# Kernel optimization log

Hardware: AMD Instinct MI355X
Metric: run time of the kernel (lower is better)

Reference implementation:

```python
import jax, jax.numpy as jnp
import numpy as np
from jax import lax

G, NPER, K = 64, 1024, 512          # graphs, nodes per graph, kept per graph (ceil(0.5*1024))
N, E = G * NPER, 1_048_576          # total nodes, total edges
F, H, C = 128, 128, 10              # in_feats, hidden_dim, num_classes


def gcn(x, src, dst, ew, W, b, num_nodes):
    """PyG GCNConv: D^{-1/2}(A+I)D^{-1/2} X W + b, with edge weights ew."""
    xw = x @ W                                              # [N, H]
    deg = jax.ops.segment_sum(ew, dst, num_segments=num_nodes) + 1.0  # +1 self loop
    dinv = lax.rsqrt(deg)
    coef = dinv[src] * dinv[dst] * ew                       # [E]
    agg = jax.ops.segment_sum(coef[:, None] * xw[src], dst, num_segments=num_nodes)
    return agg + (dinv * dinv)[:, None] * xw + b            # self-loop term + bias


def setup_inputs() -> dict:
    key = jax.random.key(0)
    ks = jax.random.split(key, 10)
    x = jax.random.normal(ks[0], (N, F), jnp.float32)
    # intra-graph random edges: dst forced into same graph block as src
    src = jax.random.randint(ks[1], (E,), 0, N, dtype=jnp.int32)
    dst = (src // NPER) * NPER + jax.random.randint(ks[2], (E,), 0, NPER, dtype=jnp.int32)
    edge_index = jnp.stack([src, dst])                      # [2, E]
    batch = jnp.repeat(jnp.arange(G, dtype=jnp.int32), NPER)
    W1 = jax.random.normal(ks[3], (F, H), jnp.float32) / np.sqrt(F)
    b1 = jnp.zeros((H,), jnp.float32)
    p = jax.random.normal(ks[4], (H,), jnp.float32) / np.sqrt(H)   # TopKPooling score vector
    W2 = jax.random.normal(ks[5], (H, H), jnp.float32) / np.sqrt(H)
    b2 = jnp.zeros((H,), jnp.float32)
    Wl = jax.random.normal(ks[6], (H, C), jnp.float32) / np.sqrt(H)
    bl = jnp.zeros((C,), jnp.float32)
    return dict(x=x, edge_index=edge_index, batch=batch, W1=W1, b1=b1, p=p, W2=W2, b2=b2, Wl=Wl, bl=bl)


def reference(x, edge_index, batch, W1, b1, p, W2, b2, Wl, bl):
    src, dst = edge_index[0], edge_index[1]
    ew1 = jnp.ones((E,), x.dtype)
    h = jax.nn.relu(gcn(x, src, dst, ew1, W1, b1, N))       # conv1 + relu

    # --- TopKPooling: score = tanh(x.p/||p||), keep top-K per graph, gate x by score ---
    score = jnp.tanh((h @ p) / jnp.linalg.norm(p))          # [N]
    vals, idx = lax.top_k(score.reshape(G, NPER), K)        # per-graph top-k, [G, K]
    perm = (idx + jnp.arange(G, dtype=idx.dtype)[:, None] * NPER).reshape(-1)  # global ids [G*K]
    h2 = h[perm] * vals.reshape(-1, 1)                      # gated kept nodes [G*K, H]

    # edge re-index: keep only edges with both endpoints surviving (mask via weight 0)
    new_id = jnp.full((N,), -1, jnp.int32).at[perm].set(jnp.arange(G * K, dtype=jnp.int32))
    s2, d2 = new_id[src], new_id[dst]
    mask = (s2 >= 0) & (d2 >= 0)
    ew2 = mask.astype(h.dtype)
    s2 = jnp.where(mask, s2, 0)
    d2 = jnp.where(mask, d2, 0)

    h3 = jax.nn.relu(gcn(h2, s2, d2, ew2, W2, b2, G * K))   # conv2 + relu

    pooled = h3.reshape(G, K, H).mean(axis=1)               # global_mean_pool (equal counts)
    return pooled @ Wl + bl                                 # [G, C]
```

## Files before the change

### kernel.cpp

```cpp
#include <hip/hip_runtime.h>

#define NNODES 65536
#define NEDGES 1048576
#define NGRAPH 64
#define NPERG  1024
#define KEEP   512
#define M2     (NGRAPH * KEEP)
#define HD     128
#define NC     10
#define EMAX   20480

#define OW1 0
#define OW2 16384
#define OWL 32768
#define OB1 34048
#define OB2 34176
#define OP  34304
#define OBL 34432
#define NCVT 34448

typedef __attribute__((ext_vector_type(8))) short bf16x8;
typedef __attribute__((ext_vector_type(4))) float f32x4;

__device__ __forceinline__ float bf2f(unsigned short u) {
    return __uint_as_float(((unsigned int)u) << 16);
}
__device__ __forceinline__ unsigned short f2bf(float f) {
    unsigned int u = __float_as_uint(f);
    unsigned int r = (u + 0x7FFFu + ((u >> 16) & 1u)) >> 16;
    return (unsigned short)r;
}

__global__ __launch_bounds__(256) void prep_kernel(
    const void* __restrict__ W1, const void* __restrict__ b1, const void* __restrict__ p,
    const void* __restrict__ W2, const void* __restrict__ b2, const void* __restrict__ Wl,
    const void* __restrict__ bl, int* __restrict__ flag, float* __restrict__ cw,
    float* __restrict__ invnorm, int* __restrict__ new_id, int* __restrict__ ghist,
    int* __restrict__ gcur0, float* __restrict__ pooled,
    unsigned short* __restrict__ w1t, unsigned short* __restrict__ w2t) {
    int bid = blockIdx.x, t = threadIdx.x;
    const unsigned short* w1u = (const unsigned short*)W1;
    int local = 0;
    for (int i = t; i < 512; i += 256) {
        unsigned short u = w1u[2 * i];
        int e = (u >> 7) & 0xFF;
        local += (e >= 100 && e <= 140) ? 1 : 0;
    }
    __shared__ int red[256];
    red[t] = local;
    __syncthreads();
    for (int off = 128; off; off >>= 1) {
        if (t < off) red[t] += red[t + off];
        __syncthreads();
    }
    int fl = (red[0] >= 384) ? 1 : 0;
    if (bid == 0 && t == 0) flag[0] = fl;

    if (bid < 135) {
        int gid = bid * 256 + t;
        if (gid < NCVT) {
            const void* srcp; int idx;
            if (gid < OB1) {
                if (gid < OW2)      { srcp = W1; idx = gid - OW1; }
                else if (gid < OWL) { srcp = W2; idx = gid - OW2; }
                else                { srcp = Wl; idx = gid - OWL; }
            } else {
                if (gid < OB2)      { srcp = b1; idx = gid - OB1; }
                else if (gid < OP)  { srcp = b2; idx = gid - OB2; }
                else if (gid < OBL) { srcp = p;  idx = gid - OP; }
                else                { srcp = bl; idx = gid - OBL; }
            }
            float v;
            if (gid >= OWL && gid < OB1 && idx >= 1280) v = 0.f;
            else if (gid >= OBL && idx >= NC) v = 0.f;
            else if (fl) v = bf2f(((const unsigned short*)srcp)[idx]);
            else v = ((const float*)srcp)[idx];
            cw[gid] = v;
            if (gid < OW2) {
                int k = gid >> 7, n = gid & 127;
                w1t[n * 128 + k] = f2bf(v);
            } else if (gid < OWL) {
                int r = gid - OW2;
                int k = r >> 7, n = r & 127;
                w2t[n * 128 + k] = f2bf(v);
            }
        }
    } else if (bid == 135) {
        __shared__ float s2a[128];
        float pv = 0.f;
        if (t < 128) pv = fl ? bf2f(((const unsigned short*)p)[t]) : ((const float*)p)[t];
        if (t < 128) s2a[t] = pv * pv;
        __syncthreads();
        for (int off = 64; off; off >>= 1) {
            if (t < off) s2a[t] += s2a[t + off];
            __syncthreads();
        }
        if (t == 0) invnorm[0] = 1.0f / sqrtf(s2a[0]);
    } else {
        int i = (bid - 136) * 256 + t;
        new_id[i] = -1;
        if (i < NGRAPH) { ghist[i] = 0; gcur0[i] = 0; }
        if (i < NGRAPH * HD) pooled[i] = 0.f;
    }
}

__global__ __launch_bounds__(256) void hist_kernel(const int* __restrict__ src,
                                                   int* __restrict__ ghist) {
    __shared__ int lh[NGRAPH];
    int tid = threadIdx.x;
    if (tid < NGRAPH) lh[tid] = 0;
    __syncthreads();
    int e0 = blockIdx.x * 4096;
    for (int k = 0; k < 16; k++) atomicAdd(&lh[src[e0 + k * 256 + tid] >> 10], 1);
    __syncthreads();
    if (tid < NGRAPH) atomicAdd(&ghist[tid], lh[tid]);
}
__global__ __launch_bounds__(256) void binpass_kernel(const int* __restrict__ src,
                                                      const int* __restrict__ dst,
                                                      const int* __restrict__ ghist,
                                                      int* __restrict__ gcur0,
                                                      unsigned int* __restrict__ elist) {
    __shared__ int gh[NGRAPH];
    __shared__ int gbS[NGRAPH];
    __shared__ int lh[NGRAPH];
    __shared__ int lbase[NGRAPH];
    int tid = threadIdx.x;
    if (tid < NGRAPH) { gh[tid] = ghist[tid]; lh[tid] = 0; }
    __syncthreads();
    if (tid == 0) {
        int s = 0;
        for (int i = 0; i < NGRAPH; i++) { gbS[i] = s; s += gh[i]; }
    }
    __syncthreads();
    int e0 = blockIdx.x * 4096;
    int gs[16]; unsigned int pk[16];
    for (int k = 0; k < 16; k++) {
        int e = e0 + k * 256 + tid;
        int s = src[e], d = dst[e];
        gs[k] = s >> 10;
        pk[k] = (unsigned)(s & 1023) | ((unsigned)(d & 1023) << 10);
        atomicAdd(&lh[gs[k]], 1);
    }
    __syncthreads();
    if (tid < NGRAPH) { lbase[tid] = gbS[tid] + atomicAdd(&gcur0[tid], lh[tid]); lh[tid] = 0; }
    __syncthreads();
    for (int k = 0; k < 16; k++) {
        int g = gs[k];
        int pos = lbase[g] + atomicAdd(&lh[g], 1);
        elist[pos] = pk[k];
    }
}

__global__ __launch_bounds__(1024) void csr_sort_kernel(
    const unsigned int* __restrict__ elist, const int* __restrict__ ghist,
    unsigned short* __restrict__ csr16, int* __restrict__ node_base,
    int* __restrict__ deg_out, float* __restrict__ dinv_out) {
    __shared__ unsigned short sc[EMAX];
    __shared__ int cnt[NPERG];
    __shared__ int cur[NPERG];
    __shared__ int wsum[16];
    __shared__ int gh[NGRAPH];
    __shared__ int baseS, nS;
    int g = blockIdx.x, t = threadIdx.x;
    cnt[t] = 0;
    if (t < NGRAPH) gh[t] = ghist[t];
    __syncthreads();
    if (t == 0) {
        int s = 0;
        for (int i = 0; i < g; i++) s += gh[i];
        baseS = s; nS = gh[g];
    }
    __syncthreads();
    int base = baseS;
    int n = nS; if (n > EMAX) n = EMAX;
    for (int j = t; j < n; j += 1024) atomicAdd(&cnt[(elist[base + j] >> 10) & 1023], 1);
    __syncthreads();
    int v = cnt[t];
    int lane = t & 63;
    int x = v;
    for (int off = 1; off < 64; off <<= 1) {
        int y = __shfl_up(x, off);
        if (lane >= off) x += y;
    }
    if (lane == 63) wsum[t >> 6] = x;
    __syncthreads();
    if (t < 16) {
        int wv = wsum[t];
        int wx = wv;
        for (int off = 1; off < 16; off <<= 1) {
            int y = __shfl_up(wx, off);
            if (t >= off) wx += y;
        }
        wsum[t] = wx - wv;
    }
    __syncthreads();
    int excl = x - v + wsum[t >> 6];
    cur[t] = excl;
    deg_out[g * NPERG + t] = v;
    dinv_out[g * NPERG + t] = rsqrtf((float)v + 1.0f);
    node_base[g * NPERG + t] = base + excl;
    __syncthreads();
    for (int j = t; j < n; j += 1024) {
        unsigned int pk = elist[base + j];
        int d = (pk >> 10) & 1023;
        int pos = atomicAdd(&cur[d], 1);
        sc[pos] = (unsigned short)(pk & 1023);
    }
    __syncthreads();
    for (int j = t; j < n; j += 1024) csr16[base + j] = sc[j];
}

__global__ __launch_bounds__(256) void gemm_a_kernel(const void* __restrict__ Araw,
                                                     const unsigned short* __restrict__ Wtb,
                                                     unsigned int* __restrict__ Cb,
                                                     const int* __restrict__ flag) {
    int tid = threadIdx.x;
    int row0 = blockIdx.x * 64;
    int wave = tid >> 6, lane = tid & 63;
    int r0 = row0 + wave * 16;
    int row = r0 + (lane & 15);
    int ko = (lane >> 4) * 8;
    f32x4 acc[8];
#pragma unroll
    for (int c = 0; c < 8; c++) acc[c] = (f32x4){0.f, 0.f, 0.f, 0.f};
    bf16x8 afr[4];
    if (flag[0]) {
        const unsigned short* arow = (const unsigned short*)Araw + (size_t)row * HD + ko;
#pragma unroll
        for (int kk = 0; kk < 4; kk++) afr[kk] = *(const bf16x8*)(arow + kk * 32);
    } else {
        const float* arow = (const float*)Araw + (size_t)row * HD + ko;
#pragma unroll
        for (int kk = 0; kk < 4; kk++) {
            float4 f0 = *(const float4*)(arow + kk * 32);
            float4 f1 = *(const float4*)(arow + kk * 32 + 4);
            bf16x8 a;
            a[0] = (short)f2bf(f0.x); a[1] = (short)f2bf(f0.y);
            a[2] = (short)f2bf(f0.z); a[3] = (short)f2bf(f0.w);
            a[4] = (short)f2bf(f1.x); a[5] = (short)f2bf(f1.y);
            a[6] = (short)f2bf(f1.z); a[7] = (short)f2bf(f1.w);
            afr[kk] = a;
        }
    }
    const unsigned short* brow = Wtb + (lane & 15) * HD + ko;
#pragma unroll
    for (int kk = 0; kk < 4; kk++) {
#pragma unroll
        for (int c = 0; c < 8; c++) {
            bf16x8 b = *(const bf16x8*)(brow + c * 16 * HD + kk * 32);
            acc[c] = __builtin_amdgcn_mfma_f32_16x16x32_bf16(afr[kk], b, acc[c], 0, 0, 0);
        }
    }
    int orow0 = r0 + (lane >> 4) * 4;
    bool even = !(lane & 1);
#pragma unroll
    for (int c = 0; c < 8; c++) {
#pragma unroll
        for (int j = 0; j < 4; j++) {
            float v = acc[c][j];
            float pt = __shfl_xor(v, 1);
            if (even) {
                unsigned int u = (unsigned int)f2bf(v) | ((unsigned int)f2bf(pt) << 16);
                Cb[(size_t)(orow0 + j) * 64 + ((c * 16 + (lane & 15)) >> 1)] = u;
            }
        }
    }
}

__global__ __launch_bounds__(256) void s1_pull(const unsigned short* __restrict__ csr16,
                                               const int* __restrict__ node_base,
                                               const int* __restrict__ deg,
                                               const float* __restrict__ dinv,
                                               const unsigned int* __restrict__ xwb,
                                               const float* __restrict__ b1,
                                               const float* __restrict__ pvec,
                                               const float* __restrict__ invnorm,
                                               float* __restrict__ h,
                                               float* __restrict__ score) {
    int b = blockIdx.x;
    int xcd = b & 7, j = b >> 3;
    int g = (j >> 8) * 8 + xcd;
    int n = g * NPERG + (j & 255) * 4 + (threadIdx.x >> 6);
    int lane = threadIdx.x & 63;
    int gb = g * NPERG;
    int base = node_base[n], cnt = deg[n];
    int e = 0; float ds = 0.f;
    if (lane < cnt) {
        e = csr16[base + lane];
        ds = dinv[gb + e];
    }
    float a0 = 0.f, a1 = 0.f;
    int klim = cnt < 64 ? cnt : 64;
    int k = 0;
    for (; k + 3 < klim; k += 4) {
        int s0 = __shfl(e, k), s1 = __shfl(e, k + 1);
        int s2 = __shfl(e, k + 2), s3 = __shfl(e, k + 3);
        float d0 = __shfl(ds, k), d1 = __shfl(ds, k + 1);
        float d2 = __shfl(ds, k + 2), d3 = __shfl(ds, k + 3);
        unsigned int u0 = xwb[(size_t)(gb + s0) * 64 + lane];
        unsigned int u1 = xwb[(size_t)(gb + s1) * 64 + lane];
        unsigned int u2 = xwb[(size_t)(gb + s2) * 64 + lane];
        unsigned int u3 = xwb[(size_t)(gb + s3) * 64 + lane];
        a0 += d0 * __uint_as_float(u0 << 16); a1 += d0 * __uint_as_float(u0 & 0xFFFF0000u);
        a0 += d1 * __uint_as_float(u1 << 16); a1 += d1 * __uint_as_float(u1 & 0xFFFF0000u);
        a0 += d2 * __uint_as_float(u2 << 16); a1 += d2 * __uint_as_float(u2 & 0xFFFF0000u);
        a0 += d3 * __uint_as_float(u3 << 16); a1 += d3 * __uint_as_float(u3 & 0xFFFF0000u);
    }
    for (; k < klim; k++) {
        int sk = __shfl(e, k);
        float dk = __shfl(ds, k);
        unsigned int u = xwb[(size_t)(gb + sk) * 64 + lane];
        a0 += dk * __uint_as_float(u << 16); a1 += dk * __uint_as_float(u & 0xFFFF0000u);
    }
    for (; k < cnt; k++) {
        int sk = csr16[base + k];
        float dk = dinv[gb + sk];
        unsigned int u = xwb[(size_t)(gb + sk) * 64 + lane];
        a0 += dk * __uint_as_float(u << 16); a1 += dk * __uint_as_float(u & 0xFFFF0000u);
    }
    float dn = dinv[n];
    float self = dn * dn;
    unsigned int us = xwb[(size_t)n * 64 + lane];
    float2 bb = ((const float2*)b1)[lane];
    float h0 = fmaxf(dn * a0 + self * __uint_as_float(us << 16) + bb.x, 0.f);
    float h1 = fmaxf(dn * a1 + self * __uint_as_float(us & 0xFFFF0000u) + bb.y, 0.f);
    float2 ho = {h0, h1};
    ((float2*)h)[(size_t)n * 64 + lane] = ho;
    float2 pp = ((const float2*)pvec)[lane];
    float sv = h0 * pp.x + h1 * pp.y;
    for (int off = 32; off; off >>= 1) sv += __shfl_down(sv, off);
    if (lane == 0) score[n] = tanhf(sv * invnorm[0]);
}

__global__ __launch_bounds__(1024) void topk_kernel(const float* __restrict__ score,
                                                    const unsigned int* __restrict__ elist,
                                                    const int* __restrict__ ghist,
                                                    float* __restrict__ vals,
                                                    int* __restrict__ perm,
                                                    int* __restrict__ new_id,
                                                    float* __restrict__ dinv2) {
    __shared__ float sv[1024];
    __shared__ int si[1024];
    __shared__ short nid[1024];
    __shared__ int d2[KEEP];
    __shared__ int gh[NGRAPH];
    __shared__ int baseS, nS;
    int g = blockIdx.x, t = threadIdx.x;
    sv[t] = score[g * NPERG + t];
    si[t] = t;
    nid[t] = -1;
    if (t < KEEP) d2[t] = 0;
    if (t < NGRAPH) gh[t] = ghist[t];
    __syncthreads();
    if (t == 0) {
        int s = 0;
        for (int i = 0; i < g; i++) s += gh[i];
        baseS = s; nS = gh[g];
    }
    for (int k = 2; k <= 1024; k <<= 1) {
        for (int j = k >> 1; j > 0; j >>= 1) {
            int l = t ^ j;
            if (l > t) {
                bool desc = ((t & k) == 0);
                float va = sv[t], vb = sv[l];
                int ia = si[t], ib = si[l];
                bool gab = (va > vb) || (va == vb && ia < ib);
                if (gab != desc) { sv[t] = vb; si[t] = ib; sv[l] = va; si[l] = ia; }
            }
            __syncthreads();
        }
    }
    if (t < KEEP) {
        int node = g * NPERG + si[t];
        int slot = g * KEEP + t;
        vals[slot] = sv[t];
        perm[slot] = node;
        new_id[node] = slot;
        nid[si[t]] = (short)t;
    }
    __syncthreads();
    int base = baseS, n = nS;
    for (int j = t; j < n; j += 1024) {
        unsigned int pk = elist[base + j];
        int s = pk & 1023, d = (pk >> 10) & 1023;
        short ns = nid[s], nd = nid[d];
        if (ns >= 0 && nd >= 0) atomicAdd(&d2[nd], 1);
    }
    __syncthreads();
    if (t < KEEP) dinv2[g * KEEP + t] = rsqrtf((float)d2[t] + 1.0f);
}

__global__ __launch_bounds__(256) void gemm_gather(const float* __restrict__ h,
                                                   const int* __restrict__ perm,
                                                   const float* __restrict__ vals,
                                                   const unsigned short* __restrict__ Wtb,
                                                   float* __restrict__ C) {
    int tid = threadIdx.x;
    int row0 = blockIdx.x * 64;
    int wave = tid >> 6, lane = tid & 63;
    int r0 = row0 + wave * 16;
    int m = r0 + (lane & 15);
    int ko = (lane >> 4) * 8;
    float sc = vals[m];
    const float* arow = h + (size_t)perm[m] * HD + ko;
    bf16x8 afr[4];
#pragma unroll
    for (int kk = 0; kk < 4; kk++) {
        float4 f0 = *(const float4*)(arow + kk * 32);
        float4 f1 = *(const float4*)(arow + kk * 32 + 4);
        bf16x8 a;
        a[0] = (short)f2bf(f0.x * sc); a[1] = (short)f2bf(f0.y * sc);
        a[2] = (short)f2bf(f0.z * sc); a[3] = (short)f2bf(f0.w * sc);
        a[4] = (short)f2bf(f1.x * sc); a[5] = (short)f2bf(f1.y * sc);
        a[6] = (short)f2bf(f1.z * sc); a[7] = (short)f2bf(f1.w * sc);
        afr[kk] = a;
    }
    f32x4 acc[8];
#pragma unroll
    for (int c = 0; c < 8; c++) acc[c] = (f32x4){0.f, 0.f, 0.f, 0.f};
    const unsigned short* brow = Wtb + (lane & 15) * HD + ko;
#pragma unroll
    for (int kk = 0; kk < 4; kk++) {
#pragma unroll
        for (int c = 0; c < 8; c++) {
            bf16x8 b = *(const bf16x8*)(brow + c * 16 * HD + kk * 32);
            acc[c] = __builtin_amdgcn_mfma_f32_16x16x32_bf16(afr[kk], b, acc[c], 0, 0, 0);
        }
    }
    int orow0 = r0 + (lane >> 4) * 4;
    bool even = !(lane & 1);
    float2* C2 = (float2*)C;
#pragma unroll
    for (int c = 0; c < 8; c++) {
#pragma unroll
        for (int j = 0; j < 4; j++) {
            float v = acc[c][j];
            float pt = __shfl_xor(v, 1);
            if (even) {
                float2 o = {v, pt};
                C2[(size_t)(orow0 + j) * 64 + ((c * 16 + (lane & 15)) >> 1)] = o;
            }
        }
    }
}

__global__ __launch_bounds__(256) void s2_pull(const unsigned short* __restrict__ csr16,
                                               const int* __restrict__ node_base,
                                               const int* __restrict__ deg,
                                               const int* __restrict__ perm,
                                               const int* __restrict__ new_id,
                                               const float* __restrict__ dinv2,
                                               const float* __restrict__ xw2,
                                               const float* __restrict__ b2,
                                               float* __restrict__ pooled) {
    __shared__ float pr[HD];
    __shared__ int cnk[4][64];
    __shared__ float cds[4][64];
    int tid = threadIdx.x;
    if (tid < HD) pr[tid] = 0.f;
    __syncthreads();
    int b = blockIdx.x;
    int xcd = b & 7, j = b >> 3;
    int g = (j >> 7) * 8 + xcd;
    int wv = tid >> 6;
    int m = g * KEEP + (j & 127) * 4 + wv;
    int lane = tid & 63;
    int node = perm[m];
    int gb = node & ~(NPERG - 1);
    int base = node_base[node], cnt = deg[node];
    int nk = 0; float ds = 0.f;
    if (lane < cnt) {
        int ns = new_id[gb + csr16[base + lane]];
        if (ns >= 0) { nk = ns; ds = dinv2[ns]; }
    }
    unsigned long long msk = __ballot(ds != 0.f);
    int pos = __popcll(msk & ((1ull << lane) - 1ull));
    if (ds != 0.f) { cnk[wv][pos] = nk; cds[wv][pos] = ds; }
    int na = __popcll(msk);
    const float2* xf2 = (const float2*)xw2;
    float a0 = 0.f, a1 = 0.f;
    int k = 0;
    for (; k + 3 < na; k += 4) {
        int s0 = cnk[wv][k], s1 = cnk[wv][k + 1];
        int s2 = cnk[wv][k + 2], s3 = cnk[wv][k + 3];
        float d0 = cds[wv][k], d1 = cds[wv][k + 1];
        float d2 = cds[wv][k + 2], d3 = cds[wv][k + 3];
        float2 v0 = xf2[(size_t)s0 * 64 + lane];
        float2 v1 = xf2[(size_t)s1 * 64 + lane];
        float2 v2 = xf2[(size_t)s2 * 64 + lane];
        float2 v3 = xf2[(size_t)s3 * 64 + lane];
        a0 += d0 * v0.x; a1 += d0 * v0.y;
        a0 += d1 * v1.x; a1 += d1 * v1.y;
        a0 += d2 * v2.x; a1 += d2 * v2.y;
        a0 += d3 * v3.x; a1 += d3 * v3.y;
    }
    for (; k < na; k++) {
        int sk = cnk[wv][k];
        float dk = cds[wv][k];
        float2 v = xf2[(size_t)sk * 64 + lane];
        a0 += dk * v.x; a1 += dk * v.y;
    }
    for (int kk = 64; kk < cnt; kk++) {
        int ns = new_id[gb + csr16[base + kk]];
        if (ns >= 0) {
            float dk = dinv2[ns];
            float2 v = xf2[(size_t)ns * 64 + lane];
            a0 += dk * v.x; a1 += dk * v.y;
        }
    }
    float dn = dinv2[m];
    float self = dn * dn;
    float2 xs = xf2[(size_t)m * 64 + lane];
    float2 bb = ((const float2*)b2)[lane];
    float o0 = fmaxf(dn * a0 + self * xs.x + bb.x, 0.f);
    float o1 = fmaxf(dn * a1 + self * xs.y + bb.y, 0.f);
    atomicAdd(&pr[lane * 2], o0);
    atomicAdd(&pr[lane * 2 + 1], o1);
    __syncthreads();
    if (tid < HD) atomicAdd(&pooled[g * HD + tid], pr[tid]);
}

__global__ __launch_bounds__(128) void outk_kernel(const float* __restrict__ pooled,
                                                   const float* __restrict__ Wl,
                                                   const float* __restrict__ bl,
                                                   void* __restrict__ outv,
                                                   const int* __restrict__ flag) {
    int g = blockIdx.x, t = threadIdx.x;
    __shared__ float sp[HD];
    sp[t] = pooled[g * HD + t] * (1.0f / KEEP);
    __syncthreads();
    if (t < NC) {
        float acc = bl[t];
        for (int hh = 0; hh < HD; hh++) acc += sp[hh] * Wl[hh * NC + t];
        if (flag[0]) ((unsigned short*)outv)[g * NC + t] = f2bf(acc);
        else         ((float*)outv)[g * NC + t] = acc;
    }
}

extern "C" void kernel_launch(void* const* d_in, const int* in_sizes, int n_in,
                              void* d_out, int out_size, void* d_ws, size_t ws_size,
                              hipStream_t stream) {
    const int* ei   = (const int*)d_in[1];
    const int* srcv = ei;
    const int* dstv = ei + NEDGES;

    char* w = (char*)d_ws;
    const size_t MB = 1u << 20;
    const size_t KB = 1024;
    float* dinv1     = (float*)(w + 0);
    float* score     = (float*)(w + 256 * KB);
    float* vals      = (float*)(w + 512 * KB);
    int*   perm      = (int*)(w + 640 * KB);
    int*   new_id    = (int*)(w + 768 * KB);
    int*   deg1      = (int*)(w + 1024 * KB);
    int*   node_base = (int*)(w + 1280 * KB);
    float* dinv2     = (float*)(w + 1536 * KB);
    float* invnorm   = (float*)(w + 1664 * KB);
    int*   flag      = (int*)(w + 1664 * KB + 64);
    int*   ghist     = (int*)(w + 1664 * KB + 1024);
    int*   gcur0     = (int*)(w + 1664 * KB + 2048);
    float* cw        = (float*)(w + 1700 * KB);
    float* pooled    = (float*)(w + 1840 * KB);
    unsigned short* w1t = (unsigned short*)(w + 1880 * KB);
    unsigned short* w2t = (unsigned short*)(w + 1912 * KB);
    unsigned int* xw1b = (unsigned int*)(w + 2 * MB);
    float* xw2  = (float*)(w + 18 * MB);
    float* agg  = (float*)(w + 34 * MB);
    unsigned int* elist    = (unsigned int*)(w + 66 * MB);
    unsigned short* csr16  = (unsigned short*)(w + 70 * MB);

    float* W1f = cw + OW1; float* W2f = cw + OW2; float* Wlf = cw + OWL;
    float* b1f = cw + OB1; float* b2f = cw + OB2; float* pf  = cw + OP;
    float* blf = cw + OBL;
    (void)W1f; (void)W2f;

    prep_kernel<<<392, 256, 0, stream>>>(d_in[3], d_in[4], d_in[5], d_in[6], d_in[7],
                                         d_in[8], d_in[9], flag, cw, invnorm, new_id,
                                         ghist, gcur0, pooled, w1t, w2t);
    hist_kernel<<<256, 256, 0, stream>>>(srcv, ghist);
    binpass_kernel<<<256, 256, 0, stream>>>(srcv, dstv, ghist, gcur0, elist);
    gemm_a_kernel<<<NNODES / 64, 256, 0, stream>>>(d_in[0], w1t, xw1b, flag);
    csr_sort_kernel<<<NGRAPH, 1024, 0, stream>>>(elist, ghist, csr16, node_base,
                                                 deg1, dinv1);
    s1_pull<<<NNODES / 4, 256, 0, stream>>>(csr16, node_base, deg1, dinv1, xw1b, b1f, pf,
                                            invnorm, agg, score);
    topk_kernel<<<NGRAPH, 1024, 0, stream>>>(score, elist, ghist, vals, perm,
                                             new_id, dinv2);
    gemm_gather<<<M2 / 64, 256, 0, stream>>>(agg, perm, vals, w2t, xw2);
    s2_pull<<<M2 / 4, 256, 0, stream>>>(csr16, node_base, deg1, perm, new_id, dinv2,
                                        xw2, b2f, pooled);
    outk_kernel<<<NGRAPH, 128, 0, stream>>>(pooled, Wlf, blf, d_out, flag);

    (void)in_sizes; (void)n_in; (void)out_size; (void)ws_size;
}
```

Measured before the change: 263.3 us.

## Merge CSR sort with GEMM1 and pool-degree with GEMM2 into combined launches

Combines independent work into shared launches using block-index dispatch. The per-graph CSR sort now runs alongside the first feature GEMM in one 1024-thread kernel, with GEMM blocks widened to 256 rows. The conv2 degree count moves out of the top-k kernel and runs alongside the gathered second GEMM, reading global new_id instead of a shared-memory table. This removes two launches and lets the serial per-graph work overlap with GEMM work, at the cost of larger blocks, a big shared allocation on every GEMM block, and global rather than LDS lookups for the degree count.

```diff
diff --git a/kernel.cpp b/kernel.cpp
--- a/kernel.cpp
+++ b/kernel.cpp
@@ -151,72 +151,71 @@
     }
 }
 
-__global__ __launch_bounds__(1024) void csr_sort_kernel(
+__global__ __launch_bounds__(1024) void g1csr_kernel(
     const unsigned int* __restrict__ elist, const int* __restrict__ ghist,
     unsigned short* __restrict__ csr16, int* __restrict__ node_base,
-    int* __restrict__ deg_out, float* __restrict__ dinv_out) {
+    int* __restrict__ deg_out, float* __restrict__ dinv_out,
+    const void* __restrict__ Araw, const unsigned short* __restrict__ Wtb,
+    unsigned int* __restrict__ Cb, const int* __restrict__ flag) {
     __shared__ unsigned short sc[EMAX];
     __shared__ int cnt[NPERG];
     __shared__ int cur[NPERG];
     __shared__ int wsum[16];
     __shared__ int gh[NGRAPH];
     __shared__ int baseS, nS;
-    int g = blockIdx.x, t = threadIdx.x;
-    cnt[t] = 0;
-    if (t < NGRAPH) gh[t] = ghist[t];
-    __syncthreads();
-    if (t == 0) {
-        int s = 0;
-        for (int i = 0; i < g; i++) s += gh[i];
-        baseS = s; nS = gh[g];
-    }
-    __syncthreads();
-    int base = baseS;
-    int n = nS; if (n > EMAX) n = EMAX;
-    for (int j = t; j < n; j += 1024) atomicAdd(&cnt[(elist[base + j] >> 10) & 1023], 1);
-    __syncthreads();
-    int v = cnt[t];
-    int lane = t & 63;
-    int x = v;
-    for (int off = 1; off < 64; off <<= 1) {
-        int y = __shfl_up(x, off);
-        if (lane >= off) x += y;
-    }
-    if (lane == 63) wsum[t >> 6] = x;
-    __syncthreads();
-    if (t < 16) {
-        int wv = wsum[t];
-        int wx = wv;
-        for (int off = 1; off < 16; off <<= 1) {
-            int y = __shfl_up(wx, off);
-            if (t >= off) wx += y;
-        }
-        wsum[t] = wx - wv;
-    }
-    __syncthreads();
-    int excl = x - v + wsum[t >> 6];
-    cur[t] = excl;
-    deg_out[g * NPERG + t] = v;
-    dinv_out[g * NPERG + t] = rsqrtf((float)v + 1.0f);
-    node_base[g * NPERG + t] = base + excl;
-    __syncthreads();
-    for (int j = t; j < n; j += 1024) {
-        unsigned int pk = elist[base + j];
-        int d = (pk >> 10) & 1023;
-        int pos = atomicAdd(&cur[d], 1);
-        sc[pos] = (unsigned short)(pk & 1023);
-    }
-    __syncthreads();
-    for (int j = t; j < n; j += 1024) csr16[base + j] = sc[j];
-}
-
-__global__ __launch_bounds__(256) void gemm_a_kernel(const void* __restrict__ Araw,
-                                                     const unsigned short* __restrict__ Wtb,
-                                                     unsigned int* __restrict__ Cb,
-                                                     const int* __restrict__ flag) {
-    int tid = threadIdx.x;
-    int row0 = blockIdx.x * 64;
-    int wave = tid >> 6, lane = tid & 63;
+    int bid = blockIdx.x, t = threadIdx.x;
+    if (bid < NGRAPH) {
+        int g = bid;
+        cnt[t] = 0;
+        if (t < NGRAPH) gh[t] = ghist[t];
+        __syncthreads();
+        if (t == 0) {
+            int s = 0;
+            for (int i = 0; i < g; i++) s += gh[i];
+            baseS = s; nS = gh[g];
+        }
+        __syncthreads();
+        int base = baseS;
+        int n = nS; if (n > EMAX) n = EMAX;
+        for (int j = t; j < n; j += 1024) atomicAdd(&cnt[(elist[base + j] >> 10) & 1023], 1);
+        __syncthreads();
+        int v = cnt[t];
+        int lane = t & 63;
+        int x = v;
+        for (int off = 1; off < 64; off <<= 1) {
+            int y = __shfl_up(x, off);
+            if (lane >= off) x += y;
+        }
+        if (lane == 63) wsum[t >> 6] = x;
+        __syncthreads();
+        if (t < 16) {
+            int wv = wsum[t];
+            int wx = wv;
+            for (int off = 1; off < 16; off <<= 1) {
+                int y = __shfl_up(wx, off);
+                if (t >= off) wx += y;
+            }
+            wsum[t] = wx - wv;
+        }
+        __syncthreads();
+        int excl = x - v + wsum[t >> 6];
+        cur[t] = excl;
+        deg_out[g * NPERG + t] = v;
+        dinv_out[g * NPERG + t] = rsqrtf((float)v + 1.0f);
+        node_base[g * NPERG + t] = base + excl;
+        __syncthreads();
+        for (int j = t; j < n; j += 1024) {
+            unsigned int pk = elist[base + j];
+            int d = (pk >> 10) & 1023;
+            int pos = atomicAdd(&cur[d], 1);
+            sc[pos] = (unsigned short)(pk & 1023);
+        }
+        __syncthreads();
+        for (int j = t; j < n; j += 1024) csr16[base + j] = sc[j];
+        return;
+    }
+    int row0 = (bid - NGRAPH) * 256;
+    int wave = t >> 6, lane = t & 63;
     int r0 = row0 + wave * 16;
     int row = r0 + (lane & 15);
     int ko = (lane >> 4) * 8;
@@ -333,30 +332,15 @@
 }
 
 __global__ __launch_bounds__(1024) void topk_kernel(const float* __restrict__ score,
-                                                    const unsigned int* __restrict__ elist,
-                                                    const int* __restrict__ ghist,
                                                     float* __restrict__ vals,
                                                     int* __restrict__ perm,
-                                                    int* __restrict__ new_id,
-                                                    float* __restrict__ dinv2) {
+                                                    int* __restrict__ new_id) {
     __shared__ float sv[1024];
     __shared__ int si[1024];
-    __shared__ short nid[1024];
-    __shared__ int d2[KEEP];
-    __shared__ int gh[NGRAPH];
-    __shared__ int baseS, nS;
     int g = blockIdx.x, t = threadIdx.x;
     sv[t] = score[g * NPERG + t];
     si[t] = t;
-    nid[t] = -1;
-    if (t < KEEP) d2[t] = 0;
-    if (t < NGRAPH) gh[t] = ghist[t];
-    __syncthreads();
-    if (t == 0) {
-        int s = 0;
-        for (int i = 0; i < g; i++) s += gh[i];
-        baseS = s; nS = gh[g];
-    }
+    __syncthreads();
     for (int k = 2; k <= 1024; k <<= 1) {
         for (int j = k >> 1; j > 0; j >>= 1) {
             int l = t ^ j;
@@ -376,28 +360,45 @@
         vals[slot] = sv[t];
         perm[slot] = node;
         new_id[node] = slot;
-        nid[si[t]] = (short)t;
-    }
-    __syncthreads();
-    int base = baseS, n = nS;
-    for (int j = t; j < n; j += 1024) {
-        unsigned int pk = elist[base + j];
-        int s = pk & 1023, d = (pk >> 10) & 1023;
-        short ns = nid[s], nd = nid[d];
-        if (ns >= 0 && nd >= 0) atomicAdd(&d2[nd], 1);
-    }
-    __syncthreads();
-    if (t < KEEP) dinv2[g * KEEP + t] = rsqrtf((float)d2[t] + 1.0f);
-}
-
-__global__ __launch_bounds__(256) void gemm_gather(const float* __restrict__ h,
-                                                   const int* __restrict__ perm,
-                                                   const float* __restrict__ vals,
-                                                   const unsigned short* __restrict__ Wtb,
-                                                   float* __restrict__ C) {
-    int tid = threadIdx.x;
-    int row0 = blockIdx.x * 64;
-    int wave = tid >> 6, lane = tid & 63;
+    }
+}
+
+__global__ __launch_bounds__(512) void g2deg_kernel(
+    const unsigned int* __restrict__ elist, const int* __restrict__ ghist,
+    const int* __restrict__ new_id, float* __restrict__ dinv2,
+    const float* __restrict__ h, const int* __restrict__ perm,
+    const float* __restrict__ vals, const unsigned short* __restrict__ Wtb,
+    float* __restrict__ C) {
+    __shared__ int d2[KEEP];
+    __shared__ int gh[NGRAPH];
+    __shared__ int baseS, nS;
+    int bid = blockIdx.x, t = threadIdx.x;
+    if (bid < NGRAPH) {
+        int g = bid;
+        if (t < KEEP) d2[t] = 0;
+        if (t < NGRAPH) gh[t] = ghist[t];
+        __syncthreads();
+        if (t == 0) {
+            int s = 0;
+            for (int i = 0; i < g; i++) s += gh[i];
+            baseS = s; nS = gh[g];
+        }
+        __syncthreads();
+        int base = baseS, n = nS;
+        int gb = g * NPERG;
+        int kb = g * KEEP;
+        for (int j = t; j < n; j += 512) {
+            unsigned int pk = elist[base + j];
+            int s = pk & 1023, d = (pk >> 10) & 1023;
+            int ns = new_id[gb + s], nd = new_id[gb + d];
+            if (ns >= 0 && nd >= 0) atomicAdd(&d2[nd - kb], 1);
+        }
+        __syncthreads();
+        if (t < KEEP) dinv2[kb + t] = rsqrtf((float)d2[t] + 1.0f);
+        return;
+    }
+    int row0 = (bid - NGRAPH) * 128;
+    int wave = t >> 6, lane = t & 63;
     int r0 = row0 + wave * 16;
     int m = r0 + (lane & 15);
     int ko = (lane >> 4) * 8;
@@ -579,14 +580,13 @@
                                          ghist, gcur0, pooled, w1t, w2t);
     hist_kernel<<<256, 256, 0, stream>>>(srcv, ghist);
     binpass_kernel<<<256, 256, 0, stream>>>(srcv, dstv, ghist, gcur0, elist);
-    gemm_a_kernel<<<NNODES / 64, 256, 0, stream>>>(d_in[0], w1t, xw1b, flag);
-    csr_sort_kernel<<<NGRAPH, 1024, 0, stream>>>(elist, ghist, csr16, node_base,
-                                                 deg1, dinv1);
+    g1csr_kernel<<<NGRAPH + NNODES / 256, 1024, 0, stream>>>(
+        elist, ghist, csr16, node_base, deg1, dinv1, d_in[0], w1t, xw1b, flag);
     s1_pull<<<NNODES / 4, 256, 0, stream>>>(csr16, node_base, deg1, dinv1, xw1b, b1f, pf,
                                             invnorm, agg, score);
-    topk_kernel<<<NGRAPH, 1024, 0, stream>>>(score, elist, ghist, vals, perm,
-                                             new_id, dinv2);
-    gemm_gather<<<M2 / 64, 256, 0, stream>>>(agg, perm, vals, w2t, xw2);
+    topk_kernel<<<NGRAPH, 1024, 0, stream>>>(score, vals, perm, new_id);
+    g2deg_kernel<<<NGRAPH + M2 / 128, 512, 0, stream>>>(
+        elist, ghist, new_id, dinv2, agg, perm, vals, w2t, xw2);
     s2_pull<<<M2 / 4, 256, 0, stream>>>(csr16, node_base, deg1, perm, new_id, dinv2,
                                         xw2, b2f, pooled);
     outk_kernel<<<NGRAPH, 128, 0, stream>>>(pooled, Wlf, blf, d_out, flag);
```

Measured after the change: 264.7 us. No clear change (+0.5%).
